# Kernel optimization log

Hardware: AMD Instinct MI355X
Metric: run time of the kernel (lower is better)

## Reference

```python
import jax, jax.numpy as jnp
import numpy as np

N = 8192
IN_DIM = 512
HID = 256


def _gcn_conv(x, adj, W, b, drop):
    # x: [N, d_in] -> [N, d_out]
    h = jnp.matmul(x, W) + b
    if drop:
        return h
    # adj_hat = adj + I; deg = rowsum(adj_hat); out = D^-1/2 adj_hat D^-1/2 h
    deg = jnp.sum(adj, axis=1) + 1.0  # +1 from identity
    dinv = jnp.where(deg > 0, deg ** -0.5, 0.0)  # [N]
    hs = dinv[:, None] * h
    agg = jnp.matmul(adj, hs) + hs  # (adj + I) @ hs without materializing adj+I
    return dinv[:, None] * agg


def _layernorm(x, gamma, beta, eps=1e-6):
    mu = jnp.mean(x, axis=-1, keepdims=True)
    var = jnp.mean((x - mu) ** 2, axis=-1, keepdims=True)
    return (x - mu) * jax.lax.rsqrt(var + eps) * gamma + beta


def setup_inputs() -> dict:
    key = jax.random.key(0)
    ks = jax.random.split(key, 6)
    x = jax.random.normal(ks[0], (N, IN_DIM), dtype=jnp.float32)
    adj = jax.random.uniform(ks[1], (N, N), dtype=jnp.float32)
    W1 = jax.random.normal(ks[2], (IN_DIM, HID), dtype=jnp.float32) * (1.0 / np.sqrt(IN_DIM))
    b1 = jax.random.normal(ks[3], (HID,), dtype=jnp.float32) * 1e-6
    W2 = jax.random.normal(ks[4], (HID, HID), dtype=jnp.float32) * (1.0 / np.sqrt(HID))
    b2 = jax.random.normal(ks[5], (HID,), dtype=jnp.float32) * 1e-6
    ln_gamma = jnp.ones((HID,), dtype=jnp.float32)
    ln_beta = jnp.zeros((HID,), dtype=jnp.float32)
    return {"x": x, "adj": adj, "W1": W1, "b1": b1, "W2": W2, "b2": b2,
            "ln_gamma": ln_gamma, "ln_beta": ln_beta, "drop": 0}


def reference(x, adj, W1, b1, W2, b2, ln_gamma, ln_beta, drop):
    h = _gcn_conv(x, adj, W1, b1, drop)
    h = jax.nn.gelu(h, approximate=False)  # torch F.gelu default = exact erf
    h = _layernorm(h, ln_gamma, ln_beta)
    # dropout -> identity (eval / deterministic baseline)
    out = _gcn_conv(h, adj, W2, b2, drop)
    return out
```

## Files before the change

kernel.cpp:

```cpp
#include <hip/hip_runtime.h>
#include <math.h>

typedef __attribute__((ext_vector_type(4))) float f32x4;
typedef __attribute__((ext_vector_type(8))) short s16x8;
typedef __attribute__((ext_vector_type(4))) short s16x4;
typedef __attribute__((ext_vector_type(2))) int i32x2;
typedef __attribute__((ext_vector_type(4))) int i32x4;

#define BM 32
#define BN 256
#define BK 64
#define LDS_TILE ((BM + BN) * BK)

#define BM2 128
#define BN2 256
#define BK2 128
#define KFULL 8192
#define ZSPLIT 4
#define KQ (KFULL / ZSPLIT)
#define ABYTES (BM2 * BK2)
#define BBYTES (BN2 * BK2)
#define BUFB (ABYTES + BBYTES)

#define SHS 2048.0f
#define S16C (64.0f / (254.0f * 2048.0f))
#define INVSHS (1.0f / 2048.0f)

__device__ __forceinline__ unsigned short f2bf(float f) {
  unsigned int u = __float_as_uint(f);
  u += 0x7fffu + ((u >> 16) & 1u);
  return (unsigned short)(u >> 16);
}
__device__ __forceinline__ float bf2f(unsigned short h) {
  unsigned int u = ((unsigned int)h) << 16;
  return __uint_as_float(u);
}
__device__ __forceinline__ int rne_i(float x) {
  return __float_as_int(x + 12582912.0f) - 0x4B400000;
}
__device__ __forceinline__ int q_hs(float v) {
  int q = rne_i(v * SHS);
  return q < -127 ? -127 : (q > 127 ? 127 : q);
}
__device__ __forceinline__ void gload16(const void* g, void* l) {
  __builtin_amdgcn_global_load_lds(
      (const __attribute__((address_space(1))) void*)g,
      (__attribute__((address_space(3))) void*)l, 16, 0, 0);
}

template <bool BF32, int EPI>
__device__ __forceinline__ void gemm_small(int bx, unsigned short* ldsb,
                                           const float* __restrict__ A,
                                           const void* __restrict__ BTp,
                                           void* __restrict__ outp,
                                           char* __restrict__ outn,
                                           int* __restrict__ colsum,
                                           const float* __restrict__ bias,
                                           const float* __restrict__ dinv,
                                           int M, int N, int K) {
  const int tid = threadIdx.x;
  const int m0 = (bx & (M / BM - 1)) * BM;
  const int n0 = (bx / (M / BM)) * BN;
  const int sr = tid >> 3;
  const int sc = (tid & 7) * 8;
  const float* Bf = (const float*)BTp;
  const unsigned short* Bh = (const unsigned short*)BTp;

  float a_t[8];
  f32x4 b_f[8][2];
  s16x8 b_h[8];

  auto stage_load = [&](int k0) {
#pragma unroll
    for (int j = 0; j < 8; ++j)
      a_t[j] = A[(size_t)(k0 + sc + j) * M + m0 + sr];
#pragma unroll
    for (int it = 0; it < 8; ++it) {
      int n = n0 + it * 32 + sr;
      if (BF32) {
        const float* p = Bf + (size_t)n * K + k0 + sc;
        b_f[it][0] = *(const f32x4*)(p);
        b_f[it][1] = *(const f32x4*)(p + 4);
      } else {
        b_h[it] = *(const s16x8*)(Bh + (size_t)n * K + k0 + sc);
      }
    }
  };

  auto stage_write = [&](int buf) {
    unsigned short* L = ldsb + buf * LDS_TILE;
    {
      s16x8 v;
#pragma unroll
      for (int j = 0; j < 8; ++j) v[j] = (short)f2bf(a_t[j]);
      int idx = (sr * BK + sc) ^ ((sr & 7) << 3);
      *(s16x8*)(L + idx) = v;
    }
#pragma unroll
    for (int it = 0; it < 8; ++it) {
      int r = it * 32 + sr;
      s16x8 w;
      if (BF32) {
#pragma unroll
        for (int j = 0; j < 8; ++j)
          w[j] = (short)f2bf(j < 4 ? b_f[it][0][j] : b_f[it][1][j - 4]);
      } else {
        w = b_h[it];
      }
      int idx = BM * BK + ((r * BK + sc) ^ ((r & 7) << 3));
      *(s16x8*)(L + idx) = w;
    }
  };

  const int lane = tid & 63;
  const int wv = tid >> 6;
  const int g = lane >> 4, lr = lane & 15;

  int aidx[2][2], bidx[4][2];
#pragma unroll
  for (int m = 0; m < 2; ++m)
#pragma unroll
    for (int ks = 0; ks < 2; ++ks) {
      int r = m * 16 + lr;
      aidx[m][ks] = (r * BK + ks * 32 + g * 8) ^ ((r & 7) << 3);
    }
#pragma unroll
  for (int n = 0; n < 4; ++n)
#pragma unroll
    for (int ks = 0; ks < 2; ++ks) {
      int r = wv * 64 + n * 16 + lr;
      bidx[n][ks] = BM * BK + ((r * BK + ks * 32 + g * 8) ^ ((r & 7) << 3));
    }

  f32x4 acc[2][4];
#pragma unroll
  for (int m = 0; m < 2; ++m)
#pragma unroll
    for (int n = 0; n < 4; ++n) {
      f32x4 z = {0.f, 0.f, 0.f, 0.f};
      acc[m][n] = z;
    }

  auto compute = [&](int buf) {
    const unsigned short* L = ldsb + buf * LDS_TILE;
    s16x8 af[2][2], bfr[4][2];
#pragma unroll
    for (int m = 0; m < 2; ++m)
#pragma unroll
      for (int ks = 0; ks < 2; ++ks) af[m][ks] = *(const s16x8*)(L + aidx[m][ks]);
#pragma unroll
    for (int n = 0; n < 4; ++n)
#pragma unroll
      for (int ks = 0; ks < 2; ++ks) bfr[n][ks] = *(const s16x8*)(L + bidx[n][ks]);
#pragma unroll
    for (int m = 0; m < 2; ++m)
#pragma unroll
      for (int n = 0; n < 4; ++n)
#pragma unroll
        for (int ks = 0; ks < 2; ++ks)
          acc[m][n] = __builtin_amdgcn_mfma_f32_16x16x32_bf16(af[m][ks], bfr[n][ks],
                                                              acc[m][n], 0, 0, 0);
  };

  stage_load(0);
  stage_write(0);
  __syncthreads();
  int cur = 0;
  const int nt = K / BK;
  for (int t = 0; t < nt; ++t) {
    if (t + 1 < nt) stage_load((t + 1) * BK);
    compute(cur);
    if (t + 1 < nt) {
      stage_write(cur ^ 1);
      __syncthreads();
      cur ^= 1;
    }
  }

  if constexpr (EPI == 3) {
#pragma unroll
    for (int m = 0; m < 2; ++m)
#pragma unroll
      for (int n = 0; n < 4; ++n) {
        int col = n0 + wv * 64 + n * 16 + lr;
#pragma unroll
        for (int r = 0; r < 4; ++r) {
          int row = m0 + m * 16 + g * 4 + r;
          ((unsigned short*)outp)[(size_t)row * N + col] = f2bf(acc[m][n][r] + bias[row]);
        }
      }
  } else {
    __syncthreads();
    char* T2 = (char*)ldsb;
    int* colA2 = (int*)((char*)ldsb + 16384);
    if (tid < 32) colA2[tid] = 0;
    __syncthreads();
    int prl[2][4];
#pragma unroll
    for (int m = 0; m < 2; ++m)
#pragma unroll
      for (int r = 0; r < 4; ++r) prl[m][r] = 0;
#pragma unroll
    for (int m = 0; m < 2; ++m)
#pragma unroll
      for (int n = 0; n < 4; ++n) {
        int cl = wv * 64 + n * 16 + lr;
        float dv = dinv[n0 + cl];
#pragma unroll
        for (int r = 0; r < 4; ++r) {
          int rl = m * 16 + g * 4 + r;
          int q = q_hs((acc[m][n][r] + bias[m0 + rl]) * dv);
          T2[cl * 48 + rl] = (char)q;
          ((char*)outp)[(size_t)(m0 + rl) * N + n0 + cl] = (char)q;
          prl[m][r] += q;
        }
      }
#pragma unroll
    for (int m = 0; m < 2; ++m)
#pragma unroll
      for (int r = 0; r < 4; ++r)
        atomicAdd(&colA2[m * 16 + g * 4 + r], prl[m][r]);
    __syncthreads();
#pragma unroll
    for (int h = 0; h < 2; ++h) {
      i32x4 vv = *(const i32x4*)(T2 + tid * 48 + h * 16);
      *(i32x4*)(outn + (size_t)(n0 + tid) * 256 + m0 + h * 16) = vv;
    }
    if (tid < 32) atomicAdd(&colsum[m0 + tid], colA2[tid]);
  }
}

__global__ __launch_bounds__(256) void prep(const float* __restrict__ adj,
                                            const float* __restrict__ x,
                                            const float* __restrict__ W1,
                                            const float* __restrict__ b1,
                                            char* __restrict__ adjq,
                                            float* __restrict__ dinv,
                                            unsigned short* __restrict__ h1,
                                            int* __restrict__ colsum1,
                                            int* __restrict__ colsum2) {
  __shared__ unsigned short lds[2 * LDS_TILE];
  int bx = blockIdx.x;
  if (bx < 256) {
    gemm_small<true, 3>(bx, lds, W1, x, h1, nullptr, nullptr, b1, nullptr, 256, 8192, 512);
    return;
  }
  bx -= 256;
  const int tid = threadIdx.x;
  if (bx == 0) {
    colsum1[tid] = 0;
    colsum2[tid] = 0;
  }
  float* smf = (float*)lds;
  float psum[2];
#pragma unroll
  for (int rr = 0; rr < 2; ++rr) {
    int row = bx * 2 + rr;
    const float* src = adj + (size_t)row * 8192;
    char* dst = adjq + (size_t)row * 8192;
    float s = 0.f;
    for (int c = tid * 8; c < 8192; c += 2048) {
      f32x4 v0 = __builtin_nontemporal_load((const f32x4*)(src + c));
      f32x4 v1 = __builtin_nontemporal_load((const f32x4*)(src + c + 4));
      s += v0[0] + v0[1] + v0[2] + v0[3] + v1[0] + v1[1] + v1[2] + v1[3];
      i32x2 o;
      o[0] = (rne_i((v0[0] - 0.5f) * 254.f) & 0xff) |
             ((rne_i((v0[1] - 0.5f) * 254.f) & 0xff) << 8) |
             ((rne_i((v0[2] - 0.5f) * 254.f) & 0xff) << 16) |
             (rne_i((v0[3] - 0.5f) * 254.f) << 24);
      o[1] = (rne_i((v1[0] - 0.5f) * 254.f) & 0xff) |
             ((rne_i((v1[1] - 0.5f) * 254.f) & 0xff) << 8) |
             ((rne_i((v1[2] - 0.5f) * 254.f) & 0xff) << 16) |
             (rne_i((v1[3] - 0.5f) * 254.f) << 24);
      *(i32x2*)(dst + c) = o;
    }
    psum[rr] = s;
  }
#pragma unroll
  for (int rr = 0; rr < 2; ++rr) {
    float s = psum[rr];
#pragma unroll
    for (int off = 32; off > 0; off >>= 1) s += __shfl_down(s, off, 64);
    if ((tid & 63) == 0) smf[rr * 4 + (tid >> 6)] = s;
  }
  __syncthreads();
  if (tid < 2) {
    float tot = smf[tid * 4] + smf[tid * 4 + 1] + smf[tid * 4 + 2] + smf[tid * 4 + 3];
    dinv[bx * 2 + tid] = rsqrtf(tot + 1.0f);
  }
}

__global__ __launch_bounds__(256) void scale_tr(const unsigned short* __restrict__ h1,
                                                const float* __restrict__ dinv,
                                                char* __restrict__ hq1,
                                                char* __restrict__ hq1n,
                                                int* __restrict__ colsum1) {
  __shared__ char Tq[64][80];
  __shared__ int colA[64];
  int nt_ = blockIdx.x >> 2, ht = blockIdx.x & 3;
  int n0 = nt_ * 64, h0 = ht * 64;
  const int tid = threadIdx.x;
  const int c8 = (tid & 7) * 8;
  if (tid < 64) colA[tid] = 0;
  __syncthreads();
  f32x4 d0 = *(const f32x4*)(dinv + n0 + c8);
  f32x4 d1 = *(const f32x4*)(dinv + n0 + c8 + 4);
#pragma unroll
  for (int it = 0; it < 2; ++it) {
    int hh = (tid >> 3) + it * 32;
    s16x8 v = *(const s16x8*)(h1 + (size_t)(h0 + hh) * 8192 + n0 + c8);
    unsigned int lo = 0, hi = 0;
    int ssum = 0;
#pragma unroll
    for (int j = 0; j < 8; ++j) {
      float dv = (j < 4) ? d0[j] : d1[j - 4];
      int q = q_hs(bf2f((unsigned short)v[j]) * dv);
      Tq[c8 + j][hh] = (char)q;
      ssum += q;
      if (j < 4) lo |= ((unsigned int)(q & 0xff)) << (8 * j);
      else       hi |= ((unsigned int)(q & 0xff)) << (8 * (j - 4));
    }
    i32x2 o;
    o[0] = (int)lo;
    o[1] = (int)hi;
    *(i32x2*)(hq1 + (size_t)(h0 + hh) * 8192 + n0 + c8) = o;
    ssum += __shfl_xor(ssum, 1, 64);
    ssum += __shfl_xor(ssum, 2, 64);
    ssum += __shfl_xor(ssum, 4, 64);
    if ((tid & 7) == 0) atomicAdd(&colA[hh], ssum);
  }
  __syncthreads();
  int node = tid >> 2, h16 = (tid & 3) * 16;
  i32x4 vv = *(const i32x4*)(&Tq[node][h16]);
  *(i32x4*)(hq1n + (size_t)(n0 + node) * 256 + h0 + h16) = vv;
  if (tid < 64) atomicAdd(&colsum1[h0 + tid], colA[tid]);
}

__global__ __launch_bounds__(512) void gemm_big(const char* __restrict__ A,
                                                const char* __restrict__ B,
                                                short* __restrict__ P16) {
  __shared__ char lds[3 * BUFB];
  const int tid = threadIdx.x;
  const int mt = blockIdx.x & 63;
  const int z = blockIdx.x >> 6;
  const int m0 = mt * BM2;

  const int trow = tid >> 3;
  const int srcgr = (tid & 7) ^ (trow & 7);

  const char* Asrc[2];
#pragma unroll
  for (int j = 0; j < 2; ++j)
    Asrc[j] = A + (size_t)(m0 + j * 64 + trow) * KFULL + (size_t)z * KQ + srcgr * 16;
  const char* Bsrc[4];
#pragma unroll
  for (int j = 0; j < 4; ++j)
    Bsrc[j] = B + (size_t)(j * 64 + trow) * KFULL + (size_t)z * KQ + srcgr * 16;

  auto stage = [&](int buf, int t) {
    char* L = lds + buf * BUFB;
#pragma unroll
    for (int j = 0; j < 2; ++j)
      gload16(Asrc[j] + (size_t)t * BK2, L + (j * 512 + tid) * 16);
#pragma unroll
    for (int j = 0; j < 4; ++j)
      gload16(Bsrc[j] + (size_t)t * BK2, L + ABYTES + (j * 512 + tid) * 16);
  };

  const int w = tid >> 6, l = tid & 63;
  const int wr = w >> 2, wc = w & 3;
  const int g = l >> 4, lr = l & 15;
  int aoff[4][2], boff[4][2];
#pragma unroll
  for (int m = 0; m < 4; ++m)
#pragma unroll
    for (int ks = 0; ks < 2; ++ks) {
      int r = wr * 64 + m * 16 + lr;
      aoff[m][ks] = r * BK2 + (((ks * 4 + g) ^ (r & 7)) * 16);
    }
#pragma unroll
  for (int n = 0; n < 4; ++n)
#pragma unroll
    for (int ks = 0; ks < 2; ++ks) {
      int r = wc * 64 + n * 16 + lr;
      boff[n][ks] = ABYTES + r * BK2 + (((ks * 4 + g) ^ (r & 7)) * 16);
    }

  i32x4 acc[4][4];
#pragma unroll
  for (int m = 0; m < 4; ++m)
#pragma unroll
    for (int n = 0; n < 4; ++n) {
      i32x4 zz = {0, 0, 0, 0};
      acc[m][n] = zz;
    }

  stage(0, 0);
  stage(1, 1);

  const int nt = KQ / BK2;
  for (int t = 0; t < nt; ++t) {
    int cur = t % 3;
    if (t + 1 < nt) asm volatile("s_waitcnt vmcnt(6)" ::: "memory");
    else            asm volatile("s_waitcnt vmcnt(0)" ::: "memory");
    asm volatile("s_barrier" ::: "memory");
    __builtin_amdgcn_sched_barrier(0);

    const char* L = lds + cur * BUFB;
    i32x4 af[4][2], bfr[4][2];
#pragma unroll
    for (int m = 0; m < 4; ++m)
#pragma unroll
      for (int ks = 0; ks < 2; ++ks) af[m][ks] = *(const i32x4*)(L + aoff[m][ks]);
#pragma unroll
    for (int n = 0; n < 4; ++n)
#pragma unroll
      for (int ks = 0; ks < 2; ++ks) bfr[n][ks] = *(const i32x4*)(L + boff[n][ks]);

    if (t + 2 < nt) stage((t + 2) % 3, t + 2);

    __builtin_amdgcn_s_setprio(1);
#pragma unroll
    for (int m = 0; m < 4; ++m)
#pragma unroll
      for (int n = 0; n < 4; ++n)
#pragma unroll
        for (int ks = 0; ks < 2; ++ks)
          acc[m][n] = __builtin_amdgcn_mfma_i32_16x16x64_i8(af[m][ks], bfr[n][ks],
                                                            acc[m][n], 0, 0, 0);
    __builtin_amdgcn_s_setprio(0);
  }

  __syncthreads();
  unsigned short* Tp = (unsigned short*)lds;
#pragma unroll
  for (int m = 0; m < 4; ++m)
#pragma unroll
    for (int n = 0; n < 4; ++n) {
      int cl = wc * 64 + n * 16 + lr;
#pragma unroll
      for (int r = 0; r < 4; ++r) {
        int rl = wr * 64 + m * 16 + g * 4 + r;
        int v = (acc[m][n][r] + 32) >> 6;
        v = v < -32768 ? -32768 : (v > 32767 ? 32767 : v);
        Tp[rl * 264 + cl] = (unsigned short)(short)v;
      }
    }
  __syncthreads();
  short* Pz = P16 + (size_t)z * 8192 * 256 + (size_t)m0 * 256;
#pragma unroll
  for (int pass = 0; pass < 8; ++pass) {
    int c = pass * 512 + tid;
    int r = c >> 5, off = (c & 31) * 8;
    s16x8 v = *(const s16x8*)(Tp + r * 264 + off);
    *(s16x8*)(Pz + (size_t)c * 8) = v;
  }
}

__global__ __launch_bounds__(256) void reduce_ln(const short* __restrict__ P16,
                                                 const char* __restrict__ hq1n,
                                                 const int* __restrict__ colsum1,
                                                 const float* __restrict__ dinv,
                                                 const float* __restrict__ gamma,
                                                 const float* __restrict__ beta,
                                                 unsigned short* __restrict__ hln) {
  const size_t ZSTR = (size_t)8192 * 256;
  int row = blockIdx.x * 4 + (threadIdx.x >> 6);
  int l = threadIdx.x & 63;
  const short* p = P16 + (size_t)row * 256 + l * 4;
  s16x4 a = *(const s16x4*)p;
  s16x4 b = *(const s16x4*)(p + ZSTR);
  s16x4 c = *(const s16x4*)(p + 2 * ZSTR);
  s16x4 d = *(const s16x4*)(p + 3 * ZSTR);
  int q4 = *(const int*)(hq1n + (size_t)row * 256 + l * 4);
  i32x4 cs = *(const i32x4*)(colsum1 + l * 4);
  float di = dinv[row];
  float gl[4];
  float s = 0.f, q = 0.f;
#pragma unroll
  for (int j = 0; j < 4; ++j) {
    float agg = (float)((int)a[j] + b[j] + c[j] + d[j]) * S16C +
                0.5f * (float)cs[j] * INVSHS +
                (float)((signed char)(q4 >> (8 * j))) * INVSHS;
    float v = agg * di;
    float gv = 0.5f * v * (1.0f + erff(v * 0.70710678118654752440f));
    gl[j] = gv;
    s += gv;
    q += gv * gv;
  }
#pragma unroll
  for (int off = 1; off < 64; off <<= 1) {
    s += __shfl_xor(s, off, 64);
    q += __shfl_xor(q, off, 64);
  }
  float mu = s * (1.0f / 256.0f);
  float var = q * (1.0f / 256.0f) - mu * mu;
  float rs = rsqrtf(fmaxf(var, 0.f) + 1e-6f);
  f32x4 gm = *(const f32x4*)(gamma + l * 4);
  f32x4 bt = *(const f32x4*)(beta + l * 4);
  unsigned short o4[4];
#pragma unroll
  for (int j = 0; j < 4; ++j)
    o4[j] = f2bf((gl[j] - mu) * rs * gm[j] + bt[j]);
  *(unsigned long long*)(hln + (size_t)row * 256 + l * 4) =
      *(const unsigned long long*)o4;
}

__global__ __launch_bounds__(256) void reduce_sc(const short* __restrict__ P16,
                                                 const char* __restrict__ hq2n,
                                                 const int* __restrict__ colsum2,
                                                 const float* __restrict__ dinv,
                                                 float* __restrict__ out) {
  const size_t ZSTR = (size_t)8192 * 256;
  int row = blockIdx.x * 4 + (threadIdx.x >> 6);
  int l = threadIdx.x & 63;
  const short* p = P16 + (size_t)row * 256 + l * 4;
  s16x4 a = *(const s16x4*)p;
  s16x4 b = *(const s16x4*)(p + ZSTR);
  s16x4 c = *(const s16x4*)(p + 2 * ZSTR);
  s16x4 d = *(const s16x4*)(p + 3 * ZSTR);
  int q4 = *(const int*)(hq2n + (size_t)row * 256 + l * 4);
  i32x4 cs = *(const i32x4*)(colsum2 + l * 4);
  float di = dinv[row];
  f32x4 o;
#pragma unroll
  for (int j = 0; j < 4; ++j) {
    float agg = (float)((int)a[j] + b[j] + c[j] + d[j]) * S16C +
                0.5f * (float)cs[j] * INVSHS +
                (float)((signed char)(q4 >> (8 * j))) * INVSHS;
    o[j] = agg * di;
  }
  *(f32x4*)(out + (size_t)row * 256 + l * 4) = o;
}

__global__ __launch_bounds__(256) void gemm6_k(const float* __restrict__ W2,
                                               const unsigned short* __restrict__ hln,
                                               char* __restrict__ hq2,
                                               char* __restrict__ hq2n,
                                               int* __restrict__ colsum2,
                                               const float* __restrict__ b2,
                                               const float* __restrict__ dinv) {
  __shared__ unsigned short lds[2 * LDS_TILE];
  gemm_small<false, 6>(blockIdx.x, lds, W2, hln, hq2, hq2n, colsum2, b2, dinv,
                       256, 8192, 256);
}

extern "C" void kernel_launch(void* const* d_in, const int* in_sizes, int n_in,
                              void* d_out, int out_size, void* d_ws, size_t ws_size,
                              hipStream_t stream) {
  (void)in_sizes; (void)n_in; (void)out_size; (void)ws_size;
  const float* x     = (const float*)d_in[0];
  const float* adj   = (const float*)d_in[1];
  const float* W1    = (const float*)d_in[2];
  const float* b1    = (const float*)d_in[3];
  const float* W2    = (const float*)d_in[4];
  const float* b2    = (const float*)d_in[5];
  const float* gamma = (const float*)d_in[6];
  const float* beta  = (const float*)d_in[7];
  float* out = (float*)d_out;

  char* ws = (char*)d_ws;
  float* dinv          = (float*)ws;
  int* colsum1         = (int*)(ws + (32 << 10));
  int* colsum2         = (int*)(ws + (36 << 10));
  unsigned short* h1   = (unsigned short*)(ws + (1 << 20));
  char* hq1            = (char*)(ws + (8 << 20));
  char* hq1n           = (char*)(ws + (10 << 20));
  unsigned short* hln  = (unsigned short*)(ws + (14 << 20));
  char* hq2            = (char*)(ws + (20 << 20));
  char* hq2n           = (char*)(ws + (24 << 20));
  short* P16           = (short*)(ws + (32 << 20));
  char* adjq           = (char*)(ws + (64 << 20));

  prep<<<4352, 256, 0, stream>>>(adj, x, W1, b1, adjq, dinv, h1, colsum1, colsum2);
  scale_tr<<<512, 256, 0, stream>>>(h1, dinv, hq1, hq1n, colsum1);
  gemm_big<<<256, 512, 0, stream>>>(adjq, hq1, P16);
  reduce_ln<<<2048, 256, 0, stream>>>(P16, hq1n, colsum1, dinv, gamma, beta, hln);
  gemm6_k<<<256, 256, 0, stream>>>(W2, hln, hq2, hq2n, colsum2, b2, dinv);
  gemm_big<<<256, 512, 0, stream>>>(adjq, hq2, P16);
  reduce_sc<<<2048, 256, 0, stream>>>(P16, hq2n, colsum2, dinv, out);
}
```

Baseline: 161.5 us.

## Fuse LayerNorm/GELU reduction with the W2 GEMM and quantize epilogue

Merges the reduce_ln kernel and the gemm6_k small GEMM into one lnW2 kernel. Each block of 32 nodes reduces the split-K partials, applies GELU and LayerNorm into an LDS slab, multiplies by the bf16-transposed W2 held in LDS using MFMA, and writes the int8 quantized outputs plus column sums. This drops a launch and the bf16 hln round trip through global memory. In exchange, every one of the 256 blocks reloads and transposes all of W2 (256x256 fp32) into LDS, and the large LDS footprint limits occupancy.

```diff
diff --git a/kernel.cpp b/kernel.cpp
--- a/kernel.cpp
+++ b/kernel.cpp
@@ -48,27 +48,20 @@
       (__attribute__((address_space(3))) void*)l, 16, 0, 0);
 }
 
-template <bool BF32, int EPI>
-__device__ __forceinline__ void gemm_small(int bx, unsigned short* ldsb,
-                                           const float* __restrict__ A,
-                                           const void* __restrict__ BTp,
-                                           void* __restrict__ outp,
-                                           char* __restrict__ outn,
-                                           int* __restrict__ colsum,
-                                           const float* __restrict__ bias,
-                                           const float* __restrict__ dinv,
-                                           int M, int N, int K) {
+__device__ __forceinline__ void gemm_small3(int bx, unsigned short* ldsb,
+                                            const float* __restrict__ A,
+                                            const float* __restrict__ Bf,
+                                            unsigned short* __restrict__ outp,
+                                            const float* __restrict__ bias,
+                                            int M, int N, int K) {
   const int tid = threadIdx.x;
   const int m0 = (bx & (M / BM - 1)) * BM;
   const int n0 = (bx / (M / BM)) * BN;
   const int sr = tid >> 3;
   const int sc = (tid & 7) * 8;
-  const float* Bf = (const float*)BTp;
-  const unsigned short* Bh = (const unsigned short*)BTp;
 
   float a_t[8];
   f32x4 b_f[8][2];
-  s16x8 b_h[8];
 
   auto stage_load = [&](int k0) {
 #pragma unroll
@@ -77,13 +70,9 @@
 #pragma unroll
     for (int it = 0; it < 8; ++it) {
       int n = n0 + it * 32 + sr;
-      if (BF32) {
-        const float* p = Bf + (size_t)n * K + k0 + sc;
-        b_f[it][0] = *(const f32x4*)(p);
-        b_f[it][1] = *(const f32x4*)(p + 4);
-      } else {
-        b_h[it] = *(const s16x8*)(Bh + (size_t)n * K + k0 + sc);
-      }
+      const float* p = Bf + (size_t)n * K + k0 + sc;
+      b_f[it][0] = *(const f32x4*)(p);
+      b_f[it][1] = *(const f32x4*)(p + 4);
     }
   };
 
@@ -100,13 +89,9 @@
     for (int it = 0; it < 8; ++it) {
       int r = it * 32 + sr;
       s16x8 w;
-      if (BF32) {
-#pragma unroll
-        for (int j = 0; j < 8; ++j)
-          w[j] = (short)f2bf(j < 4 ? b_f[it][0][j] : b_f[it][1][j - 4]);
-      } else {
-        w = b_h[it];
-      }
+#pragma unroll
+      for (int j = 0; j < 8; ++j)
+        w[j] = (short)f2bf(j < 4 ? b_f[it][0][j] : b_f[it][1][j - 4]);
       int idx = BM * BK + ((r * BK + sc) ^ ((r & 7) << 3));
       *(s16x8*)(L + idx) = w;
     }
@@ -177,57 +162,17 @@
     }
   }
 
-  if constexpr (EPI == 3) {
-#pragma unroll
-    for (int m = 0; m < 2; ++m)
-#pragma unroll
-      for (int n = 0; n < 4; ++n) {
-        int col = n0 + wv * 64 + n * 16 + lr;
-#pragma unroll
-        for (int r = 0; r < 4; ++r) {
-          int row = m0 + m * 16 + g * 4 + r;
-          ((unsigned short*)outp)[(size_t)row * N + col] = f2bf(acc[m][n][r] + bias[row]);
-        }
+#pragma unroll
+  for (int m = 0; m < 2; ++m)
+#pragma unroll
+    for (int n = 0; n < 4; ++n) {
+      int col = n0 + wv * 64 + n * 16 + lr;
+#pragma unroll
+      for (int r = 0; r < 4; ++r) {
+        int row = m0 + m * 16 + g * 4 + r;
+        outp[(size_t)row * N + col] = f2bf(acc[m][n][r] + bias[row]);
       }
-  } else {
-    __syncthreads();
-    char* T2 = (char*)ldsb;
-    int* colA2 = (int*)((char*)ldsb + 16384);
-    if (tid < 32) colA2[tid] = 0;
-    __syncthreads();
-    int prl[2][4];
-#pragma unroll
-    for (int m = 0; m < 2; ++m)
-#pragma unroll
-      for (int r = 0; r < 4; ++r) prl[m][r] = 0;
-#pragma unroll
-    for (int m = 0; m < 2; ++m)
-#pragma unroll
-      for (int n = 0; n < 4; ++n) {
-        int cl = wv * 64 + n * 16 + lr;
-        float dv = dinv[n0 + cl];
-#pragma unroll
-        for (int r = 0; r < 4; ++r) {
-          int rl = m * 16 + g * 4 + r;
-          int q = q_hs((acc[m][n][r] + bias[m0 + rl]) * dv);
-          T2[cl * 48 + rl] = (char)q;
-          ((char*)outp)[(size_t)(m0 + rl) * N + n0 + cl] = (char)q;
-          prl[m][r] += q;
-        }
-      }
-#pragma unroll
-    for (int m = 0; m < 2; ++m)
-#pragma unroll
-      for (int r = 0; r < 4; ++r)
-        atomicAdd(&colA2[m * 16 + g * 4 + r], prl[m][r]);
-    __syncthreads();
-#pragma unroll
-    for (int h = 0; h < 2; ++h) {
-      i32x4 vv = *(const i32x4*)(T2 + tid * 48 + h * 16);
-      *(i32x4*)(outn + (size_t)(n0 + tid) * 256 + m0 + h * 16) = vv;
-    }
-    if (tid < 32) atomicAdd(&colsum[m0 + tid], colA2[tid]);
-  }
+    }
 }
 
 __global__ __launch_bounds__(256) void prep(const float* __restrict__ adj,
@@ -242,7 +187,7 @@
   __shared__ unsigned short lds[2 * LDS_TILE];
   int bx = blockIdx.x;
   if (bx < 256) {
-    gemm_small<true, 3>(bx, lds, W1, x, h1, nullptr, nullptr, b1, nullptr, 256, 8192, 512);
+    gemm_small3(bx, lds, W1, x, h1, b1, 256, 8192, 512);
     return;
   }
   bx -= 256;
@@ -457,53 +402,146 @@
   }
 }
 
-__global__ __launch_bounds__(256) void reduce_ln(const short* __restrict__ P16,
-                                                 const char* __restrict__ hq1n,
-                                                 const int* __restrict__ colsum1,
-                                                 const float* __restrict__ dinv,
-                                                 const float* __restrict__ gamma,
-                                                 const float* __restrict__ beta,
-                                                 unsigned short* __restrict__ hln) {
+__global__ __launch_bounds__(256) void lnW2(const short* __restrict__ P16,
+                                            const char* __restrict__ hq1n,
+                                            const int* __restrict__ colsum1,
+                                            const float* __restrict__ dinv,
+                                            const float* __restrict__ gamma,
+                                            const float* __restrict__ beta,
+                                            const float* __restrict__ W2,
+                                            const float* __restrict__ b2,
+                                            char* __restrict__ hq2,
+                                            char* __restrict__ hq2n,
+                                            int* __restrict__ colsum2) {
+  __shared__ unsigned short smem[(256 + 32) * 264];
+  __shared__ int colA[256];
+  unsigned short* Wt = smem;
+  unsigned short* slab = smem + 256 * 264;
+  const int tid = threadIdx.x;
+  const int n0 = blockIdx.x * 32;
+  const int l = tid & 63;
+
+  colA[tid] = 0;
+
+  for (int i = 0; i < 64; ++i) {
+    int flat = (i * 256 + tid) * 4;
+    f32x4 v = *(const f32x4*)(W2 + flat);
+    int k = flat >> 8;
+    int h0 = flat & 255;
+#pragma unroll
+    for (int j = 0; j < 4; ++j)
+      Wt[(h0 + j) * 264 + k] = f2bf(v[j]);
+  }
+
   const size_t ZSTR = (size_t)8192 * 256;
-  int row = blockIdx.x * 4 + (threadIdx.x >> 6);
-  int l = threadIdx.x & 63;
-  const short* p = P16 + (size_t)row * 256 + l * 4;
-  s16x4 a = *(const s16x4*)p;
-  s16x4 b = *(const s16x4*)(p + ZSTR);
-  s16x4 c = *(const s16x4*)(p + 2 * ZSTR);
-  s16x4 d = *(const s16x4*)(p + 3 * ZSTR);
-  int q4 = *(const int*)(hq1n + (size_t)row * 256 + l * 4);
-  i32x4 cs = *(const i32x4*)(colsum1 + l * 4);
-  float di = dinv[row];
-  float gl[4];
-  float s = 0.f, q = 0.f;
-#pragma unroll
-  for (int j = 0; j < 4; ++j) {
-    float agg = (float)((int)a[j] + b[j] + c[j] + d[j]) * S16C +
-                0.5f * (float)cs[j] * INVSHS +
-                (float)((signed char)(q4 >> (8 * j))) * INVSHS;
-    float v = agg * di;
-    float gv = 0.5f * v * (1.0f + erff(v * 0.70710678118654752440f));
-    gl[j] = gv;
-    s += gv;
-    q += gv * gv;
-  }
-#pragma unroll
-  for (int off = 1; off < 64; off <<= 1) {
-    s += __shfl_xor(s, off, 64);
-    q += __shfl_xor(q, off, 64);
-  }
-  float mu = s * (1.0f / 256.0f);
-  float var = q * (1.0f / 256.0f) - mu * mu;
-  float rs = rsqrtf(fmaxf(var, 0.f) + 1e-6f);
   f32x4 gm = *(const f32x4*)(gamma + l * 4);
   f32x4 bt = *(const f32x4*)(beta + l * 4);
-  unsigned short o4[4];
-#pragma unroll
-  for (int j = 0; j < 4; ++j)
-    o4[j] = f2bf((gl[j] - mu) * rs * gm[j] + bt[j]);
-  *(unsigned long long*)(hln + (size_t)row * 256 + l * 4) =
-      *(const unsigned long long*)o4;
+  i32x4 cs = *(const i32x4*)(colsum1 + l * 4);
+  for (int it = 0; it < 8; ++it) {
+    int row_l = it * 4 + (tid >> 6);
+    int row = n0 + row_l;
+    const short* p = P16 + (size_t)row * 256 + l * 4;
+    s16x4 a = *(const s16x4*)p;
+    s16x4 b = *(const s16x4*)(p + ZSTR);
+    s16x4 c = *(const s16x4*)(p + 2 * ZSTR);
+    s16x4 d = *(const s16x4*)(p + 3 * ZSTR);
+    int q4 = *(const int*)(hq1n + (size_t)row * 256 + l * 4);
+    float di = dinv[row];
+    float gl[4];
+    float s = 0.f, q = 0.f;
+#pragma unroll
+    for (int j = 0; j < 4; ++j) {
+      float agg = (float)((int)a[j] + b[j] + c[j] + d[j]) * S16C +
+                  0.5f * (float)cs[j] * INVSHS +
+                  (float)((signed char)(q4 >> (8 * j))) * INVSHS;
+      float v = agg * di;
+      float gv = 0.5f * v * (1.0f + erff(v * 0.70710678118654752440f));
+      gl[j] = gv;
+      s += gv;
+      q += gv * gv;
+    }
+#pragma unroll
+    for (int off = 1; off < 64; off <<= 1) {
+      s += __shfl_xor(s, off, 64);
+      q += __shfl_xor(q, off, 64);
+    }
+    float mu = s * (1.0f / 256.0f);
+    float var = q * (1.0f / 256.0f) - mu * mu;
+    float rs = rsqrtf(fmaxf(var, 0.f) + 1e-6f);
+#pragma unroll
+    for (int j = 0; j < 4; ++j)
+      slab[row_l * 264 + l * 4 + j] = f2bf((gl[j] - mu) * rs * gm[j] + bt[j]);
+  }
+  __syncthreads();
+
+  const int w = tid >> 6;
+  const int g = l >> 4, lr = l & 15;
+  f32x4 acc[4][2];
+#pragma unroll
+  for (int mf = 0; mf < 4; ++mf)
+#pragma unroll
+    for (int nf = 0; nf < 2; ++nf) {
+      f32x4 z = {0.f, 0.f, 0.f, 0.f};
+      acc[mf][nf] = z;
+    }
+#pragma unroll
+  for (int ks = 0; ks < 8; ++ks) {
+    s16x8 bq[2];
+#pragma unroll
+    for (int nf = 0; nf < 2; ++nf)
+      bq[nf] = *(const s16x8*)(slab + (nf * 16 + lr) * 264 + ks * 32 + g * 8);
+#pragma unroll
+    for (int mf = 0; mf < 4; ++mf) {
+      s16x8 aq = *(const s16x8*)(Wt + (w * 64 + mf * 16 + lr) * 264 + ks * 32 + g * 8);
+#pragma unroll
+      for (int nf = 0; nf < 2; ++nf)
+        acc[mf][nf] = __builtin_amdgcn_mfma_f32_16x16x32_bf16(aq, bq[nf], acc[mf][nf],
+                                                              0, 0, 0);
+    }
+  }
+  __syncthreads();
+
+  char* Tt = (char*)smem;
+  char* T2 = (char*)smem + 12288;
+  float di2[2];
+#pragma unroll
+  for (int nf = 0; nf < 2; ++nf) di2[nf] = dinv[n0 + nf * 16 + lr];
+#pragma unroll
+  for (int mf = 0; mf < 4; ++mf)
+#pragma unroll
+    for (int r = 0; r < 4; ++r) {
+      int hp = w * 64 + mf * 16 + g * 4 + r;
+      float bias = b2[hp];
+      int s2 = 0;
+#pragma unroll
+      for (int nf = 0; nf < 2; ++nf) {
+        int node_l = nf * 16 + lr;
+        int qv = q_hs((acc[mf][nf][r] + bias) * di2[nf]);
+        Tt[hp * 48 + node_l] = (char)qv;
+        T2[node_l * 272 + hp] = (char)qv;
+        s2 += qv;
+      }
+      s2 += __shfl_xor(s2, 1, 64);
+      s2 += __shfl_xor(s2, 2, 64);
+      s2 += __shfl_xor(s2, 4, 64);
+      s2 += __shfl_xor(s2, 8, 64);
+      if (lr == 0) atomicAdd(&colA[hp], s2);
+    }
+  __syncthreads();
+  {
+    i32x4 v0 = *(const i32x4*)(Tt + tid * 48);
+    i32x4 v1 = *(const i32x4*)(Tt + tid * 48 + 16);
+    *(i32x4*)(hq2 + (size_t)tid * 8192 + n0) = v0;
+    *(i32x4*)(hq2 + (size_t)tid * 8192 + n0 + 16) = v1;
+  }
+  {
+    int node = tid >> 3, ch = (tid & 7) * 32;
+    i32x4 u0 = *(const i32x4*)(T2 + node * 272 + ch);
+    i32x4 u1 = *(const i32x4*)(T2 + node * 272 + ch + 16);
+    *(i32x4*)(hq2n + (size_t)(n0 + node) * 256 + ch) = u0;
+    *(i32x4*)(hq2n + (size_t)(n0 + node) * 256 + ch + 16) = u1;
+  }
+  atomicAdd(&colsum2[tid], colA[tid]);
 }
 
 __global__ __launch_bounds__(256) void reduce_sc(const short* __restrict__ P16,
@@ -533,18 +571,6 @@
   *(f32x4*)(out + (size_t)row * 256 + l * 4) = o;
 }
 
-__global__ __launch_bounds__(256) void gemm6_k(const float* __restrict__ W2,
-                                               const unsigned short* __restrict__ hln,
-                                               char* __restrict__ hq2,
-                                               char* __restrict__ hq2n,
-                                               int* __restrict__ colsum2,
-                                               const float* __restrict__ b2,
-                                               const float* __restrict__ dinv) {
-  __shared__ unsigned short lds[2 * LDS_TILE];
-  gemm_small<false, 6>(blockIdx.x, lds, W2, hln, hq2, hq2n, colsum2, b2, dinv,
-                       256, 8192, 256);
-}
-
 extern "C" void kernel_launch(void* const* d_in, const int* in_sizes, int n_in,
                               void* d_out, int out_size, void* d_ws, size_t ws_size,
                               hipStream_t stream) {
@@ -566,7 +592,6 @@
   unsigned short* h1   = (unsigned short*)(ws + (1 << 20));
   char* hq1            = (char*)(ws + (8 << 20));
   char* hq1n           = (char*)(ws + (10 << 20));
-  unsigned short* hln  = (unsigned short*)(ws + (14 << 20));
   char* hq2            = (char*)(ws + (20 << 20));
   char* hq2n           = (char*)(ws + (24 << 20));
   short* P16           = (short*)(ws + (32 << 20));
@@ -575,8 +600,8 @@
   prep<<<4352, 256, 0, stream>>>(adj, x, W1, b1, adjq, dinv, h1, colsum1, colsum2);
   scale_tr<<<512, 256, 0, stream>>>(h1, dinv, hq1, hq1n, colsum1);
   gemm_big<<<256, 512, 0, stream>>>(adjq, hq1, P16);
-  reduce_ln<<<2048, 256, 0, stream>>>(P16, hq1n, colsum1, dinv, gamma, beta, hln);
-  gemm6_k<<<256, 256, 0, stream>>>(W2, hln, hq2, hq2n, colsum2, b2, dinv);
+  lnW2<<<256, 256, 0, stream>>>(P16, hq1n, colsum1, dinv, gamma, beta, W2, b2,
+                                hq2, hq2n, colsum2);
   gemm_big<<<256, 512, 0, stream>>>(adjq, hq2, P16);
   reduce_sc<<<2048, 256, 0, stream>>>(P16, hq2n, colsum2, dinv, out);
 }
```

New measurement: 175.6 us. 8.7% more time.
